# Kernel tuning notes

Hardware: AMD Instinct MI355X
Metric: run time of the kernel (lower is better)

## Reference

```python
import jax, jax.numpy as jnp
import numpy as np

N = 50000
E = 1_600_000
IN_C = 128
HID = 128
HEADS = 4
F_OUT = HID // HEADS  # 32
NEG_SLOPE = 0.2


def _glorot(key, shape):
    fan_in, fan_out = shape[0], shape[-1]
    lim = jnp.sqrt(6.0 / (fan_in + fan_out)).astype(jnp.float32)
    return jax.random.uniform(key, shape, jnp.float32, -lim, lim)


def setup_inputs() -> dict:
    key = jax.random.key(0)
    ks = jax.random.split(key, 12)
    x = jax.random.normal(ks[0], (N, IN_C), jnp.float32)
    edge_index = jax.random.randint(ks[1], (2, E), 0, N, jnp.int32)
    # layer 0 params
    W0 = _glorot(ks[2], (IN_C, HEADS * F_OUT))
    att_src0 = _glorot(ks[3], (HEADS, F_OUT))
    att_dst0 = _glorot(ks[4], (HEADS, F_OUT))
    b0 = jnp.zeros((HEADS * F_OUT,), jnp.float32)
    # layer 1 params
    W1 = _glorot(ks[5], (HID, HEADS * F_OUT))
    att_src1 = _glorot(ks[6], (HEADS, F_OUT))
    att_dst1 = _glorot(ks[7], (HEADS, F_OUT))
    b1 = jnp.zeros((HEADS * F_OUT,), jnp.float32)
    return {"x": x, "edge_index": edge_index,
            "W0": W0, "att_src0": att_src0, "att_dst0": att_dst0, "b0": b0,
            "W1": W1, "att_src1": att_src1, "att_dst1": att_dst1, "b1": b1}


def gat_conv(x, src, dst, W, att_src, att_dst, b):
    n = x.shape[0]
    h = (x @ W).reshape(n, HEADS, F_OUT)              # [N,H,F]
    a_s = jnp.einsum('nhf,hf->nh', h, att_src)        # [N,H]
    a_d = jnp.einsum('nhf,hf->nh', h, att_dst)        # [N,H]
    e = jax.nn.leaky_relu(a_s[src] + a_d[dst], NEG_SLOPE)   # [E,H]
    # segment softmax over destination-node neighborhoods
    e_max = jax.ops.segment_max(e, dst, num_segments=n)     # [N,H]
    e_exp = jnp.exp(e - e_max[dst])                          # [E,H]
    denom = jax.ops.segment_sum(e_exp, dst, num_segments=n)  # [N,H]
    denom = jnp.where(denom > 0, denom, 1.0)
    alpha = e_exp / denom[dst]                               # [E,H]
    msg = alpha[:, :, None] * h[src]                         # [E,H,F]
    out = jax.ops.segment_sum(msg, dst, num_segments=n)      # [N,H,F]
    return out.reshape(n, HEADS * F_OUT) + b


def reference(x, edge_index, W0, att_src0, att_dst0, b0, W1, att_src1, att_dst1, b1):
    src, dst = edge_index[0], edge_index[1]
    h = gat_conv(x, src, dst, W0, att_src0, att_dst0, b0)
    h = jax.nn.relu(h)  # dropout p=0.0 / eval mode -> identity
    out = gat_conv(h, src, dst, W1, att_src1, att_dst1, b1)
    return out
```

## Files before the change

### kernel.cpp

```cpp
#include <hip/hip_runtime.h>
#include <hip/hip_fp16.h>

#define N_NODES 50000
#define N_EDGES 1600000
#define NB 196
#define NBLK 256
#define CHUNK (N_EDGES / NBLK)
#define SCAN_N (NB * NBLK)
#define GEMM_BLOCKS 256

typedef _Float16 half8_t __attribute__((ext_vector_type(8)));
typedef _Float16 half2_t __attribute__((ext_vector_type(2)));
typedef float floatx4 __attribute__((ext_vector_type(4)));

#if defined(__has_builtin)
#  if __has_builtin(__builtin_amdgcn_fdot2)
#    define HAS_FDOT2 1
#  endif
#endif
#ifndef HAS_FDOT2
#  define HAS_FDOT2 0
#endif

__global__ __launch_bounds__(256) void gemm_mfma(const float* __restrict__ Xf,
                                                 const __half* __restrict__ Xh,
                                                 int in_half,
                                                 const float* __restrict__ W,
                                                 const float* __restrict__ att_s,
                                                 const float* __restrict__ att_d,
                                                 __half* __restrict__ H16,
                                                 float* __restrict__ as_out,
                                                 float* __restrict__ ad_out, int nrows,
                                                 const int* __restrict__ hist_dst,
                                                 int* __restrict__ hist_counts) {
    __shared__ __align__(16) char lds[49152];
    int t = threadIdx.x;
    if (hist_counts != nullptr && blockIdx.x >= GEMM_BLOCKS) {
        int* hist = reinterpret_cast<int*>(lds);
        int b = blockIdx.x - GEMM_BLOCKS;
        for (int i = t; i < NB; i += 256) hist[i] = 0;
        __syncthreads();
        int s = b * CHUNK;
        for (int i = t; i < CHUNK; i += 256)
            atomicAdd(&hist[hist_dst[s + i] >> 8], 1);
        __syncthreads();
        for (int i = t; i < NB; i += 256) hist_counts[i * NBLK + b] = hist[i];
        return;
    }
    char* Alds = lds;
    char* Wlds = lds + 16384;
    int lane = t & 63, wv_ = t >> 6;
    for (int p = 0; p < 16; ++p) {
        int flat = p * 256 + t;
        int k = flat >> 5;
        int n0 = (flat & 31) * 4;
        float4 wv = reinterpret_cast<const float4*>(W)[flat];
        const float* wf = reinterpret_cast<const float*>(&wv);
        #pragma unroll
        for (int i = 0; i < 4; ++i) {
            int n = n0 + i;
            int byte = (n * 256 + k * 2) ^ ((n & 7) << 4);
            *reinterpret_cast<__half*>(Wlds + byte) = __float2half(wf[i]);
        }
    }
    int col16 = lane & 15;
    float Asv[8], Adv[8];
    #pragma unroll
    for (int nt = 0; nt < 8; ++nt) {
        Asv[nt] = att_s[nt * 16 + col16];
        Adv[nt] = att_d[nt * 16 + col16];
    }
    int ksub = (lane >> 4) * 16;
    int rloc = wv_ * 16 + col16;
    int ntiles = (nrows + 63) / 64;
    for (int tile = blockIdx.x; tile < ntiles; tile += GEMM_BLOCKS) {
        int row0 = tile * 64;
        __syncthreads();
        for (int p = 0; p < 8; ++p) {
            int r = p * 8 + (t >> 5);
            int f4 = t & 31;
            int rr = row0 + r;
            uint2 hv = make_uint2(0, 0);
            if (rr < nrows) {
                if (in_half) {
                    hv = *reinterpret_cast<const uint2*>(Xh + (size_t)rr * 128 + f4 * 4);
                } else {
                    float4 xv = reinterpret_cast<const float4*>(Xf)[(size_t)rr * 32 + f4];
                    __half2* hp = reinterpret_cast<__half2*>(&hv);
                    hp[0] = __floats2half2_rn(xv.x, xv.y);
                    hp[1] = __floats2half2_rn(xv.z, xv.w);
                }
            }
            int byte = (r * 256 + f4 * 8) ^ ((r & 7) << 4);
            *reinterpret_cast<uint2*>(Alds + byte) = hv;
        }
        __syncthreads();
        half8_t afr[4];
        #pragma unroll
        for (int kb = 0; kb < 4; ++kb) {
            int byte = (rloc * 256 + kb * 64 + ksub) ^ ((rloc & 7) << 4);
            afr[kb] = *reinterpret_cast<half8_t*>(Alds + byte);
        }
        floatx4 acc[8];
        #pragma unroll
        for (int nt = 0; nt < 8; ++nt) {
            int n = nt * 16 + col16;
            floatx4 a = {0.f, 0.f, 0.f, 0.f};
            #pragma unroll
            for (int kb = 0; kb < 4; ++kb) {
                int byte = (n * 256 + kb * 64 + ksub) ^ ((n & 7) << 4);
                half8_t bfr = *reinterpret_cast<half8_t*>(Wlds + byte);
                a = __builtin_amdgcn_mfma_f32_16x16x32_f16(afr[kb], bfr, a, 0, 0, 0);
            }
            acc[nt] = a;
        }
        float ps[4][4], pd[4][4];
        #pragma unroll
        for (int reg = 0; reg < 4; ++reg)
            #pragma unroll
            for (int h = 0; h < 4; ++h) {
                ps[reg][h] = acc[2*h][reg] * Asv[2*h] + acc[2*h+1][reg] * Asv[2*h+1];
                pd[reg][h] = acc[2*h][reg] * Adv[2*h] + acc[2*h+1][reg] * Adv[2*h+1];
            }
        #pragma unroll
        for (int m = 1; m <= 8; m <<= 1)
            #pragma unroll
            for (int reg = 0; reg < 4; ++reg)
                #pragma unroll
                for (int h = 0; h < 4; ++h) {
                    ps[reg][h] += __shfl_xor(ps[reg][h], m);
                    pd[reg][h] += __shfl_xor(pd[reg][h], m);
                }
        int rbase = row0 + wv_ * 16 + (lane >> 4) * 4;
        #pragma unroll
        for (int reg = 0; reg < 4; ++reg) {
            int grow = rbase + reg;
            if (grow < nrows) {
                #pragma unroll
                for (int nt = 0; nt < 8; ++nt)
                    H16[(size_t)grow * 128 + nt * 16 + col16] = __float2half(acc[nt][reg]);
                if (col16 == 0) {
                    *reinterpret_cast<float4*>(as_out + (size_t)grow * 4) =
                        make_float4(ps[reg][0], ps[reg][1], ps[reg][2], ps[reg][3]);
                    *reinterpret_cast<float4*>(ad_out + (size_t)grow * 4) =
                        make_float4(pd[reg][0], pd[reg][1], pd[reg][2], pd[reg][3]);
                }
            }
        }
    }
}

__global__ __launch_bounds__(1024) void scan_all(const int* __restrict__ counts,
                                                 int* __restrict__ start) {
    __shared__ int sh[1024];
    int t = threadIdx.x;
    int base = t * 49;
    int sum = 0;
    for (int i = 0; i < 49; ++i) sum += counts[base + i];
    sh[t] = sum;
    __syncthreads();
    for (int off = 1; off < 1024; off <<= 1) {
        int v = (t >= off) ? sh[t - off] : 0;
        __syncthreads();
        sh[t] += v;
        __syncthreads();
    }
    int run = sh[t] - sum;
    for (int i = 0; i < 49; ++i) {
        int c = counts[base + i];
        start[base + i] = run;
        run += c;
    }
}

__global__ __launch_bounds__(1024) void bucket_scatter(const int* __restrict__ src,
                                                       const int* __restrict__ dst,
                                                       const int* __restrict__ start,
                                                       int* __restrict__ bucketed) {
    __shared__ int cur[NB];
    int t = threadIdx.x, b = blockIdx.x;
    if (t < NB) cur[t] = start[t * NBLK + b];
    __syncthreads();
    int s = b * CHUNK;
    for (int i = t; i < CHUNK; i += 1024) {
        int d = dst[s + i];
        int p = atomicAdd(&cur[d >> 8], 1);
        bucketed[p] = (src[s + i] << 8) | (d & 255);
    }
}

__global__ __launch_bounds__(1024) void bucket_sort(const int* __restrict__ bucketed,
                                                    const int* __restrict__ start,
                                                    int* __restrict__ sorted_packed,
                                                    int* __restrict__ off) {
    __shared__ int cnt[256], scn[256], cur[256];
    int t = threadIdx.x, k = blockIdx.x;
    int base = start[k * NBLK];
    int end = (k + 1 < NB) ? start[(k + 1) * NBLK] : N_EDGES;
    int m = end - base;
    if (t < 256) cnt[t] = 0;
    __syncthreads();
    for (int i = t; i < m; i += 1024)
        atomicAdd(&cnt[bucketed[base + i] & 255], 1);
    __syncthreads();
    if (t < 256) scn[t] = cnt[t];
    __syncthreads();
    for (int o = 1; o < 256; o <<= 1) {
        int v = (t < 256 && t >= o) ? scn[t - o] : 0;
        __syncthreads();
        if (t < 256) scn[t] += v;
        __syncthreads();
    }
    if (t < 256) {
        int excl = scn[t] - cnt[t];
        cur[t] = base + excl;
        int node = k * 256 + t;
        if (node <= N_NODES) off[node] = base + excl;
    }
    __syncthreads();
    for (int i = t; i < m; i += 1024) {
        int rec = bucketed[base + i];
        int p = atomicAdd(&cur[rec & 255], 1);
        sorted_packed[p] = rec;
    }
}

__global__ __launch_bounds__(256) void gat_aggregate_v2(const __half* __restrict__ H16,
                                                        const int* __restrict__ off,
                                                        const int* __restrict__ packed,
                                                        const float* __restrict__ asb,
                                                        const float* __restrict__ adb,
                                                        const float* __restrict__ bias,
                                                        float* __restrict__ OUTF,
                                                        __half* __restrict__ OUTH,
                                                        int n, int mode) {
    int wid = (blockIdx.x * 256 + threadIdx.x) >> 6;
    int lane = threadIdx.x & 63;
    if (wid >= n) return;
    int s = off[wid], e = off[wid + 1];
    int q = lane >> 4;
    int sub = lane & 15;
    int head4 = (sub >> 2) * 4;
    int sub16 = sub * 16;
    float adv = adb[(size_t)wid * 4 + (sub >> 2)];
    const char* Hc = reinterpret_cast<const char*>(H16);
    const char* Ac = reinterpret_cast<const char*>(asb);
    float acc[8] = {0, 0, 0, 0, 0, 0, 0, 0};
    float den = 0.f;
    if (s < e) {
        int ia = s + q, ib = ia + 4;
        int ja = ia < e ? ia : s, jb = ib < e ? ib : s;
        int ra = packed[ja] & 0xFFFFFF00;
        int rb = packed[jb] & 0xFFFFFF00;
        float sa = *reinterpret_cast<const float*>(Ac + (ra >> 4) + head4);
        float sb = *reinterpret_cast<const float*>(Ac + (rb >> 4) + head4);
        for (int i = s; i < e; i += 8) {
            uint4 ha = *reinterpret_cast<const uint4*>(Hc + ra + sub16);
            uint4 hb = *reinterpret_cast<const uint4*>(Hc + rb + sub16);
            bool va = (i + q) < e, vb = (i + q + 4) < e;
            float ea = sa + adv; ea = fmaxf(ea, 0.2f * ea);
            float eb = sb + adv; eb = fmaxf(eb, 0.2f * eb);
            float wa = va ? __expf(ea) : 0.f;
            float wb = vb ? __expf(eb) : 0.f;
            int ia2 = i + 8 + q, ib2 = ia2 + 4;
            int ja2 = ia2 < e ? ia2 : s, jb2 = ib2 < e ? ib2 : s;
            ra = packed[ja2] & 0xFFFFFF00;
            rb = packed[jb2] & 0xFFFFFF00;
            sa = *reinterpret_cast<const float*>(Ac + (ra >> 4) + head4);
            sb = *reinterpret_cast<const float*>(Ac + (rb >> 4) + head4);
            den += wa + wb;
#if HAS_FDOT2
            half2_t w01 = __builtin_bit_cast(half2_t, __builtin_amdgcn_cvt_pkrtz(wa, wb));
            const uint* hau = reinterpret_cast<const uint*>(&ha);
            const uint* hbu = reinterpret_cast<const uint*>(&hb);
            #pragma unroll
            for (int j = 0; j < 4; ++j) {
                uint p0 = __builtin_amdgcn_perm(hbu[j], hau[j], 0x05040100u);
                uint p1 = __builtin_amdgcn_perm(hbu[j], hau[j], 0x07060302u);
                acc[2*j]   = __builtin_amdgcn_fdot2(__builtin_bit_cast(half2_t, p0), w01, acc[2*j],   false);
                acc[2*j+1] = __builtin_amdgcn_fdot2(__builtin_bit_cast(half2_t, p1), w01, acc[2*j+1], false);
            }
#else
            const __half2* pa = reinterpret_cast<const __half2*>(&ha);
            const __half2* pb = reinterpret_cast<const __half2*>(&hb);
            #pragma unroll
            for (int j = 0; j < 4; ++j) {
                float2 fa = __half22float2(pa[j]);
                float2 fb = __half22float2(pb[j]);
                acc[2*j]   += wa * fa.x + wb * fb.x;
                acc[2*j+1] += wa * fa.y + wb * fb.y;
            }
#endif
        }
    }
    #pragma unroll
    for (int j = 0; j < 8; ++j) acc[j] += __shfl_xor(acc[j], 16);
    den += __shfl_xor(den, 16);
    #pragma unroll
    for (int j = 0; j < 8; ++j) acc[j] += __shfl_xor(acc[j], 32);
    den += __shfl_xor(den, 32);
    if (q == 0) {
        float inv = den > 0.f ? 1.f / den : 0.f;
        float4 b0 = *reinterpret_cast<const float4*>(bias + sub * 8);
        float4 b1 = *reinterpret_cast<const float4*>(bias + sub * 8 + 4);
        float o[8];
        o[0] = acc[0]*inv + b0.x; o[1] = acc[1]*inv + b0.y;
        o[2] = acc[2]*inv + b0.z; o[3] = acc[3]*inv + b0.w;
        o[4] = acc[4]*inv + b1.x; o[5] = acc[5]*inv + b1.y;
        o[6] = acc[6]*inv + b1.z; o[7] = acc[7]*inv + b1.w;
        if (mode) {
            uint4 u;
            __half2* up = reinterpret_cast<__half2*>(&u);
            #pragma unroll
            for (int j = 0; j < 4; ++j)
                up[j] = __floats2half2_rn(fmaxf(o[2*j], 0.f), fmaxf(o[2*j+1], 0.f));
            *reinterpret_cast<uint4*>(OUTH + (size_t)wid * 128 + sub * 8) = u;
        } else {
            *reinterpret_cast<float4*>(OUTF + (size_t)wid * 128 + sub * 8) =
                make_float4(o[0], o[1], o[2], o[3]);
            *reinterpret_cast<float4*>(OUTF + (size_t)wid * 128 + sub * 8 + 4) =
                make_float4(o[4], o[5], o[6], o[7]);
        }
    }
}

extern "C" void kernel_launch(void* const* d_in, const int* in_sizes, int n_in,
                              void* d_out, int out_size, void* d_ws, size_t ws_size,
                              hipStream_t stream) {
    const float* x        = (const float*)d_in[0];
    const int*   edge     = (const int*)d_in[1];
    const float* W0       = (const float*)d_in[2];
    const float* att_src0 = (const float*)d_in[3];
    const float* att_dst0 = (const float*)d_in[4];
    const float* b0       = (const float*)d_in[5];
    const float* W1       = (const float*)d_in[6];
    const float* att_src1 = (const float*)d_in[7];
    const float* att_dst1 = (const float*)d_in[8];
    const float* b1       = (const float*)d_in[9];
    const int* src = edge;
    const int* dst = edge + N_EDGES;
    float* out = (float*)d_out;

    char* ws = (char*)d_ws;
    size_t o = 0;
    auto alloc = [&](size_t bytes) { char* p = ws + o; o += (bytes + 255) & ~(size_t)255; return p; };
    __half* H16   = (__half*)alloc((size_t)N_NODES * 128 * 2);
    float* asb    = (float*)alloc((size_t)N_NODES * 4 * 4);
    float* adb    = (float*)alloc((size_t)N_NODES * 4 * 4);
    int*   off    = (int*)alloc((size_t)(N_NODES + 1) * 4);
    int*   sorted = (int*)alloc((size_t)N_EDGES * 4);
    size_t mark = o;
    int*   counts = (int*)alloc((size_t)SCAN_N * 4);
    int*   start  = (int*)alloc((size_t)SCAN_N * 4);
    int*   bucketed = (int*)alloc((size_t)N_EDGES * 4);
    __half* h1_16 = (__half*)(ws + mark);

    int agg_blocks = N_NODES / 4;

    gemm_mfma<<<GEMM_BLOCKS + NBLK, 256, 0, stream>>>(x, (const __half*)nullptr, 0,
                                                      W0, att_src0, att_dst0,
                                                      H16, asb, adb, N_NODES, dst, counts);
    scan_all<<<1, 1024, 0, stream>>>(counts, start);
    bucket_scatter<<<NBLK, 1024, 0, stream>>>(src, dst, start, bucketed);
    bucket_sort<<<NB, 1024, 0, stream>>>(bucketed, start, sorted, off);

    gat_aggregate_v2<<<agg_blocks, 256, 0, stream>>>(H16, off, sorted, asb, adb, b0,
                                                     (float*)nullptr, h1_16, N_NODES, 1);

    gemm_mfma<<<GEMM_BLOCKS, 256, 0, stream>>>((const float*)nullptr, h1_16, 1,
                                               W1, att_src1, att_dst1,
                                               H16, asb, adb, N_NODES,
                                               (const int*)nullptr, (int*)nullptr);
    gat_aggregate_v2<<<agg_blocks, 256, 0, stream>>>(H16, off, sorted, asb, adb, b1,
                                                     out, (__half*)nullptr, N_NODES, 0);
}
```

Before: 212.9 us.

## Replace per-block bucket scan with global atomics and local LDS sort; unroll aggregation

```diff
diff --git a/kernel.cpp b/kernel.cpp
--- a/kernel.cpp
+++ b/kernel.cpp
@@ -6,7 +6,6 @@
 #define NB 196
 #define NBLK 256
 #define CHUNK (N_EDGES / NBLK)
-#define SCAN_N (NB * NBLK)
 #define GEMM_BLOCKS 256
 
 typedef _Float16 half8_t __attribute__((ext_vector_type(8)));
@@ -32,10 +31,10 @@
                                                  float* __restrict__ as_out,
                                                  float* __restrict__ ad_out, int nrows,
                                                  const int* __restrict__ hist_dst,
-                                                 int* __restrict__ hist_counts) {
+                                                 int* __restrict__ hist_totals) {
     __shared__ __align__(16) char lds[49152];
     int t = threadIdx.x;
-    if (hist_counts != nullptr && blockIdx.x >= GEMM_BLOCKS) {
+    if (hist_totals != nullptr && blockIdx.x >= GEMM_BLOCKS) {
         int* hist = reinterpret_cast<int*>(lds);
         int b = blockIdx.x - GEMM_BLOCKS;
         for (int i = t; i < NB; i += 256) hist[i] = 0;
@@ -44,7 +43,8 @@
         for (int i = t; i < CHUNK; i += 256)
             atomicAdd(&hist[hist_dst[s + i] >> 8], 1);
         __syncthreads();
-        for (int i = t; i < NB; i += 256) hist_counts[i * NBLK + b] = hist[i];
+        for (int i = t; i < NB; i += 256)
+            if (hist[i]) atomicAdd(&hist_totals[i], hist[i]);
         return;
     }
     char* Alds = lds;
@@ -150,56 +150,88 @@
     }
 }
 
-__global__ __launch_bounds__(1024) void scan_all(const int* __restrict__ counts,
-                                                 int* __restrict__ start) {
-    __shared__ int sh[1024];
-    int t = threadIdx.x;
-    int base = t * 49;
-    int sum = 0;
-    for (int i = 0; i < 49; ++i) sum += counts[base + i];
-    sh[t] = sum;
-    __syncthreads();
-    for (int off = 1; off < 1024; off <<= 1) {
-        int v = (t >= off) ? sh[t - off] : 0;
-        __syncthreads();
-        sh[t] += v;
-        __syncthreads();
-    }
-    int run = sh[t] - sum;
-    for (int i = 0; i < 49; ++i) {
-        int c = counts[base + i];
-        start[base + i] = run;
-        run += c;
-    }
-}
-
 __global__ __launch_bounds__(1024) void bucket_scatter(const int* __restrict__ src,
                                                        const int* __restrict__ dst,
-                                                       const int* __restrict__ start,
+                                                       const int* __restrict__ btotal,
+                                                       int* __restrict__ bcursor,
                                                        int* __restrict__ bucketed) {
-    __shared__ int cur[NB];
+    __shared__ int bexcl[NB];
+    __shared__ int hist[NB];
+    __shared__ int lstart[NB];
+    __shared__ int curL[NB];
+    __shared__ int gbase[NB];
+    __shared__ int recs[CHUNK];
+    __shared__ int srt[CHUNK];
     int t = threadIdx.x, b = blockIdx.x;
-    if (t < NB) cur[t] = start[t * NBLK + b];
-    __syncthreads();
-    int s = b * CHUNK;
+    int myTot = 0;
+    if (t < NB) { myTot = btotal[t]; bexcl[t] = myTot; }
+    for (int i = t; i < NB; i += 1024) hist[i] = 0;
+    __syncthreads();
+    for (int o = 1; o < NB; o <<= 1) {
+        int v = (t < NB && t >= o) ? bexcl[t - o] : 0;
+        __syncthreads();
+        if (t < NB) bexcl[t] += v;
+        __syncthreads();
+    }
+    if (t < NB) bexcl[t] -= myTot;
+    int s0 = b * CHUNK;
     for (int i = t; i < CHUNK; i += 1024) {
-        int d = dst[s + i];
-        int p = atomicAdd(&cur[d >> 8], 1);
-        bucketed[p] = (src[s + i] << 8) | (d & 255);
+        unsigned sv = (unsigned)src[s0 + i], dv = (unsigned)dst[s0 + i];
+        recs[i] = (int)((sv << 16) | dv);
+        atomicAdd(&hist[dv >> 8], 1);
+    }
+    __syncthreads();
+    int myCnt = (t < NB) ? hist[t] : 0;
+    if (t < NB) lstart[t] = myCnt;
+    __syncthreads();
+    for (int o = 1; o < NB; o <<= 1) {
+        int v = (t < NB && t >= o) ? lstart[t - o] : 0;
+        __syncthreads();
+        if (t < NB) lstart[t] += v;
+        __syncthreads();
+    }
+    if (t < NB) {
+        int ex = lstart[t] - myCnt;
+        lstart[t] = ex;
+        curL[t] = ex;
+        gbase[t] = bexcl[t] + atomicAdd(&bcursor[t], myCnt);
+    }
+    __syncthreads();
+    for (int i = t; i < CHUNK; i += 1024) {
+        int r = recs[i];
+        int bk = (int)(((unsigned)r & 0xFFFFu) >> 8);
+        int p = atomicAdd(&curL[bk], 1);
+        srt[p] = r;
+    }
+    __syncthreads();
+    for (int p = t; p < CHUNK; p += 1024) {
+        int r = srt[p];
+        unsigned d = (unsigned)r & 0xFFFFu;
+        int bk = (int)(d >> 8);
+        int g = gbase[bk] + (p - lstart[bk]);
+        bucketed[g] = (int)((((unsigned)r >> 16) << 8) | (d & 255u));
     }
 }
 
 __global__ __launch_bounds__(1024) void bucket_sort(const int* __restrict__ bucketed,
-                                                    const int* __restrict__ start,
+                                                    const int* __restrict__ btotal,
                                                     int* __restrict__ sorted_packed,
                                                     int* __restrict__ off) {
+    __shared__ int bb[NB];
     __shared__ int cnt[256], scn[256], cur[256];
     int t = threadIdx.x, k = blockIdx.x;
-    int base = start[k * NBLK];
-    int end = (k + 1 < NB) ? start[(k + 1) * NBLK] : N_EDGES;
+    if (t < NB) bb[t] = btotal[t];
+    if (t < 256) cnt[t] = 0;
+    __syncthreads();
+    for (int o = 1; o < NB; o <<= 1) {
+        int v = (t < NB && t >= o) ? bb[t - o] : 0;
+        __syncthreads();
+        if (t < NB) bb[t] += v;
+        __syncthreads();
+    }
+    int base = (k == 0) ? 0 : bb[k - 1];
+    int end  = bb[k];
     int m = end - base;
-    if (t < 256) cnt[t] = 0;
-    __syncthreads();
     for (int i = t; i < m; i += 1024)
         atomicAdd(&cnt[bucketed[base + i] & 255], 1);
     __syncthreads();
@@ -225,7 +257,7 @@
     }
 }
 
-__global__ __launch_bounds__(256) void gat_aggregate_v2(const __half* __restrict__ H16,
+__global__ __launch_bounds__(256) void gat_aggregate_v3(const __half* __restrict__ H16,
                                                         const int* __restrict__ off,
                                                         const int* __restrict__ packed,
                                                         const float* __restrict__ asb,
@@ -248,47 +280,64 @@
     float acc[8] = {0, 0, 0, 0, 0, 0, 0, 0};
     float den = 0.f;
     if (s < e) {
-        int ia = s + q, ib = ia + 4;
-        int ja = ia < e ? ia : s, jb = ib < e ? ib : s;
-        int ra = packed[ja] & 0xFFFFFF00;
-        int rb = packed[jb] & 0xFFFFFF00;
-        float sa = *reinterpret_cast<const float*>(Ac + (ra >> 4) + head4);
-        float sb = *reinterpret_cast<const float*>(Ac + (rb >> 4) + head4);
-        for (int i = s; i < e; i += 8) {
-            uint4 ha = *reinterpret_cast<const uint4*>(Hc + ra + sub16);
-            uint4 hb = *reinterpret_cast<const uint4*>(Hc + rb + sub16);
-            bool va = (i + q) < e, vb = (i + q + 4) < e;
-            float ea = sa + adv; ea = fmaxf(ea, 0.2f * ea);
-            float eb = sb + adv; eb = fmaxf(eb, 0.2f * eb);
-            float wa = va ? __expf(ea) : 0.f;
-            float wb = vb ? __expf(eb) : 0.f;
-            int ia2 = i + 8 + q, ib2 = ia2 + 4;
-            int ja2 = ia2 < e ? ia2 : s, jb2 = ib2 < e ? ib2 : s;
-            ra = packed[ja2] & 0xFFFFFF00;
-            rb = packed[jb2] & 0xFFFFFF00;
-            sa = *reinterpret_cast<const float*>(Ac + (ra >> 4) + head4);
-            sb = *reinterpret_cast<const float*>(Ac + (rb >> 4) + head4);
-            den += wa + wb;
+        int idx[4]; float sc[4];
+        #pragma unroll
+        for (int u = 0; u < 4; ++u) {
+            int ii = s + q + u * 4;
+            int jj = ii < e ? ii : s;
+            idx[u] = packed[jj] & 0xFFFFFF00;
+            sc[u] = *reinterpret_cast<const float*>(Ac + (idx[u] >> 4) + head4);
+        }
+        for (int i = s; i < e; i += 16) {
+            uint4 h0 = *reinterpret_cast<const uint4*>(Hc + idx[0] + sub16);
+            uint4 h1 = *reinterpret_cast<const uint4*>(Hc + idx[1] + sub16);
+            uint4 h2 = *reinterpret_cast<const uint4*>(Hc + idx[2] + sub16);
+            uint4 h3 = *reinterpret_cast<const uint4*>(Hc + idx[3] + sub16);
+            float w[4];
+            #pragma unroll
+            for (int u = 0; u < 4; ++u) {
+                float ev = sc[u] + adv; ev = fmaxf(ev, 0.2f * ev);
+                w[u] = (i + q + u * 4 < e) ? __expf(ev) : 0.f;
+            }
+            #pragma unroll
+            for (int u = 0; u < 4; ++u) {
+                int ii = i + 16 + q + u * 4;
+                int jj = ii < e ? ii : s;
+                idx[u] = packed[jj] & 0xFFFFFF00;
+                sc[u] = *reinterpret_cast<const float*>(Ac + (idx[u] >> 4) + head4);
+            }
+            den += (w[0] + w[1]) + (w[2] + w[3]);
 #if HAS_FDOT2
-            half2_t w01 = __builtin_bit_cast(half2_t, __builtin_amdgcn_cvt_pkrtz(wa, wb));
-            const uint* hau = reinterpret_cast<const uint*>(&ha);
-            const uint* hbu = reinterpret_cast<const uint*>(&hb);
+            half2_t w01 = __builtin_bit_cast(half2_t, __builtin_amdgcn_cvt_pkrtz(w[0], w[1]));
+            half2_t w23 = __builtin_bit_cast(half2_t, __builtin_amdgcn_cvt_pkrtz(w[2], w[3]));
+            const uint* a0 = reinterpret_cast<const uint*>(&h0);
+            const uint* a1 = reinterpret_cast<const uint*>(&h1);
+            const uint* a2 = reinterpret_cast<const uint*>(&h2);
+            const uint* a3 = reinterpret_cast<const uint*>(&h3);
             #pragma unroll
             for (int j = 0; j < 4; ++j) {
-                uint p0 = __builtin_amdgcn_perm(hbu[j], hau[j], 0x05040100u);
-                uint p1 = __builtin_amdgcn_perm(hbu[j], hau[j], 0x07060302u);
-                acc[2*j]   = __builtin_amdgcn_fdot2(__builtin_bit_cast(half2_t, p0), w01, acc[2*j],   false);
-                acc[2*j+1] = __builtin_amdgcn_fdot2(__builtin_bit_cast(half2_t, p1), w01, acc[2*j+1], false);
+                uint p0 = __builtin_amdgcn_perm(a1[j], a0[j], 0x05040100u);
+                uint p1 = __builtin_amdgcn_perm(a1[j], a0[j], 0x07060302u);
+                uint r0 = __builtin_amdgcn_perm(a3[j], a2[j], 0x05040100u);
+                uint r1 = __builtin_amdgcn_perm(a3[j], a2[j], 0x07060302u);
+                acc[2*j]   = __builtin_amdgcn_fdot2(__builtin_bit_cast(half2_t, p0), w01,
+                             __builtin_amdgcn_fdot2(__builtin_bit_cast(half2_t, r0), w23, acc[2*j],   false), false);
+                acc[2*j+1] = __builtin_amdgcn_fdot2(__builtin_bit_cast(half2_t, p1), w01,
+                             __builtin_amdgcn_fdot2(__builtin_bit_cast(half2_t, r1), w23, acc[2*j+1], false), false);
             }
 #else
-            const __half2* pa = reinterpret_cast<const __half2*>(&ha);
-            const __half2* pb = reinterpret_cast<const __half2*>(&hb);
+            const __half2* pa = reinterpret_cast<const __half2*>(&h0);
+            const __half2* pb = reinterpret_cast<const __half2*>(&h1);
+            const __half2* pc = reinterpret_cast<const __half2*>(&h2);
+            const __half2* pd_ = reinterpret_cast<const __half2*>(&h3);
             #pragma unroll
             for (int j = 0; j < 4; ++j) {
                 float2 fa = __half22float2(pa[j]);
                 float2 fb = __half22float2(pb[j]);
-                acc[2*j]   += wa * fa.x + wb * fb.x;
-                acc[2*j+1] += wa * fa.y + wb * fb.y;
+                float2 fc = __half22float2(pc[j]);
+                float2 fd = __half22float2(pd_[j]);
+                acc[2*j]   += w[0] * fa.x + w[1] * fb.x + w[2] * fc.x + w[3] * fd.x;
+                acc[2*j+1] += w[0] * fa.y + w[1] * fb.y + w[2] * fc.y + w[3] * fd.y;
             }
 #endif
         }
@@ -350,27 +399,28 @@
     int*   off    = (int*)alloc((size_t)(N_NODES + 1) * 4);
     int*   sorted = (int*)alloc((size_t)N_EDGES * 4);
     size_t mark = o;
-    int*   counts = (int*)alloc((size_t)SCAN_N * 4);
-    int*   start  = (int*)alloc((size_t)SCAN_N * 4);
+    int*   btot2    = (int*)alloc((size_t)2 * NB * 4);
     int*   bucketed = (int*)alloc((size_t)N_EDGES * 4);
     __half* h1_16 = (__half*)(ws + mark);
+    int* btotal  = btot2;
+    int* bcursor = btot2 + NB;
 
     int agg_blocks = N_NODES / 4;
 
+    hipMemsetAsync(btot2, 0, (size_t)2 * NB * 4, stream);
     gemm_mfma<<<GEMM_BLOCKS + NBLK, 256, 0, stream>>>(x, (const __half*)nullptr, 0,
                                                       W0, att_src0, att_dst0,
-                                                      H16, asb, adb, N_NODES, dst, counts);
-    scan_all<<<1, 1024, 0, stream>>>(counts, start);
-    bucket_scatter<<<NBLK, 1024, 0, stream>>>(src, dst, start, bucketed);
-    bucket_sort<<<NB, 1024, 0, stream>>>(bucketed, start, sorted, off);
-
-    gat_aggregate_v2<<<agg_blocks, 256, 0, stream>>>(H16, off, sorted, asb, adb, b0,
+                                                      H16, asb, adb, N_NODES, dst, btotal);
+    bucket_scatter<<<NBLK, 1024, 0, stream>>>(src, dst, btotal, bcursor, bucketed);
+    bucket_sort<<<NB, 1024, 0, stream>>>(bucketed, btotal, sorted, off);
+
+    gat_aggregate_v3<<<agg_blocks, 256, 0, stream>>>(H16, off, sorted, asb, adb, b0,
                                                      (float*)nullptr, h1_16, N_NODES, 1);
 
     gemm_mfma<<<GEMM_BLOCKS, 256, 0, stream>>>((const float*)nullptr, h1_16, 1,
                                                W1, att_src1, att_dst1,
                                                H16, asb, adb, N_NODES,
                                                (const int*)nullptr, (int*)nullptr);
-    gat_aggregate_v2<<<agg_blocks, 256, 0, stream>>>(H16, off, sorted, asb, adb, b1,
+    gat_aggregate_v3<<<agg_blocks, 256, 0, stream>>>(H16, off, sorted, asb, adb, b1,
                                                      out, (__half*)nullptr, N_NODES, 0);
 }
```

Result: faster. 202.8 us (-4.7%).
